# Kernel tuning notes

Measured on AMD Instinct MI355X. Metric: run time of the kernel, lower is better.

The kernel has to match this reference:

```python
import jax, jax.numpy as jnp
import numpy as np

N = 100000   # nodes
E = 1600000  # edges
IN = 768     # in_dim
H = 128      # hidden_dim
G = 64       # graphs per batch


def setup_inputs() -> dict:
    key = jax.random.key(0)
    ks = jax.random.split(key, 9)
    x = jax.random.normal(ks[0], (N, IN), jnp.float32)
    edge_index = jax.random.randint(ks[1], (2, E), 0, N, dtype=jnp.int64)
    batch = jnp.sort(jax.random.randint(ks[2], (N,), 0, G, dtype=jnp.int64))
    W1 = jax.random.normal(ks[3], (IN, H), jnp.float32) / np.float32(np.sqrt(IN))
    b1 = jax.random.normal(ks[4], (H,), jnp.float32) * 0.01
    W2 = jax.random.normal(ks[5], (H, H), jnp.float32) / np.float32(np.sqrt(H))
    b2 = jax.random.normal(ks[6], (H,), jnp.float32) * 0.01
    Wh = jax.random.normal(ks[7], (H, 2), jnp.float32) / np.float32(np.sqrt(H))
    bh = jax.random.normal(ks[8], (2,), jnp.float32) * 0.01
    return dict(x=x, edge_index=edge_index, batch=batch, W1=W1, b1=b1,
                W2=W2, b2=b2, Wh=Wh, bh=bh, num_graphs=G)


def gcn_conv(x, src, dst, W, b, n):
    # PyG GCNConv default: add self-loops (already in src/dst), symmetric norm.
    deg = jax.ops.segment_sum(jnp.ones_like(dst, x.dtype), dst, num_segments=n)
    dis = jnp.where(deg > 0, jax.lax.rsqrt(deg), jnp.zeros_like(deg))
    h = x @ W                                   # [n, out]
    norm = (dis[src] * dis[dst])[:, None]       # [E+n, 1]
    out = jax.ops.segment_sum(h[src] * norm, dst, num_segments=n)
    return out + b


def reference(x, edge_index, batch, W1, b1, W2, b2, Wh, bh, num_graphs):
    n = x.shape[0]
    loop = jnp.arange(n, dtype=edge_index.dtype)
    src = jnp.concatenate([edge_index[0], loop])
    dst = jnp.concatenate([edge_index[1], loop])
    h = jax.nn.relu(gcn_conv(x, src, dst, W1, b1, n))   # dropout = eval identity
    h = jax.nn.relu(gcn_conv(h, src, dst, W2, b2, n))
    summed = jax.ops.segment_sum(h, batch, num_segments=num_graphs)
    counts = jax.ops.segment_sum(jnp.ones((n, 1), h.dtype), batch, num_segments=num_graphs)
    emb = summed / jnp.maximum(counts, 1.0)             # global_mean_pool
    return emb @ Wh + bh
```

## Files before the change

kernel.cpp:

```cpp
#include <hip/hip_runtime.h>
#include <hip/hip_bf16.h>
#include <hip/hip_fp16.h>

static constexpr int N_NODES  = 100000;
static constexpr int N_EDGES  = 1600000;
static constexpr int DIM_IN   = 768;
static constexpr int DIM_H    = 128;
static constexpr int N_GRAPHS = 64;
static constexpr int NB_SCAN  = (N_NODES + 255) / 256;

typedef __attribute__((ext_vector_type(8))) _Float16 half8;
typedef __attribute__((ext_vector_type(4))) float f32x4;

__global__ void k_indeg(const int* __restrict__ edst, int* __restrict__ indeg) {
    int e = blockIdx.x * 256 + threadIdx.x;
    if (e < N_EDGES) atomicAdd(&indeg[edst[e]], 1);
}

__global__ void k_convW(const float* __restrict__ W1, const float* __restrict__ W2,
                        _Float16* __restrict__ W1t, _Float16* __restrict__ W2t) {
    int i = blockIdx.x * 256 + threadIdx.x;
    const int total1 = DIM_IN * DIM_H;
    if (i < total1) {
        int k = i >> 7, n = i & 127;
        W1t[(size_t)n * DIM_IN + k] = (_Float16)W1[i];
    } else if (i < total1 + DIM_H * DIM_H) {
        int j = i - total1;
        int k = j >> 7, n = j & 127;
        W2t[(size_t)n * DIM_H + k] = (_Float16)W2[j];
    }
}

__global__ void k_scan1(const int* __restrict__ indeg, int* __restrict__ rp,
                        int* __restrict__ bsum, float* __restrict__ dis) {
    __shared__ int s[256];
    int t = threadIdx.x;
    int i = blockIdx.x * 256 + t;
    int v = (i < N_NODES) ? indeg[i] : 0;
    s[t] = v;
    __syncthreads();
    for (int off = 1; off < 256; off <<= 1) {
        int x = (t >= off) ? s[t - off] : 0;
        __syncthreads();
        s[t] += x;
        __syncthreads();
    }
    if (i < N_NODES) {
        rp[i] = s[t] - v;
        dis[i] = rsqrtf((float)v + 1.0f);
    }
    if (t == 255) bsum[blockIdx.x] = s[255];
}

__global__ void k_scan2(int* __restrict__ bsum, const int* __restrict__ batch,
                        int* __restrict__ gstart) {
    __shared__ int s[512];
    int t = threadIdx.x;
    int v = (t < NB_SCAN) ? bsum[t] : 0;
    s[t] = v;
    __syncthreads();
    for (int off = 1; off < 512; off <<= 1) {
        int x = (t >= off) ? s[t - off] : 0;
        __syncthreads();
        s[t] += x;
        __syncthreads();
    }
    if (t < NB_SCAN) bsum[t] = s[t] - v;
    if (t <= N_GRAPHS) {
        int lo = 0, hi = N_NODES;
        while (lo < hi) {
            int mid = (lo + hi) >> 1;
            if (batch[mid] < t) lo = mid + 1; else hi = mid;
        }
        gstart[t] = lo;
    }
}

__global__ void k_scatter(const int* __restrict__ esrc, const int* __restrict__ edst,
                          const int* __restrict__ rp, const int* __restrict__ bsum,
                          const float* __restrict__ dis,
                          int* __restrict__ cursor, uint2* __restrict__ csrw) {
    int e = blockIdx.x * 256 + threadIdx.x;
    if (e >= N_EDGES) return;
    int d = edst[e];
    int sv = esrc[e];
    int pos = atomicAdd(&cursor[d], 1);
    uint2 val;
    val.x = (uint)sv;
    val.y = __float_as_uint(dis[sv]);
    csrw[rp[d] + bsum[d >> 8] + pos] = val;
}

#define LDSTR 40

template<int K, bool AFP32>
__global__ __launch_bounds__(256) void k_gemm_mfma(const void* __restrict__ Av,
                                                   const _Float16* __restrict__ Wt,
                                                   _Float16* __restrict__ C,
                                                   int nrows) {
    __shared__ ushort As[128 * LDSTR];
    __shared__ ushort Bs[128 * LDSTR];

    const int t = threadIdx.x;
    const int row0 = blockIdx.x * 128;
    const int srow = t >> 1;
    const int skoff = (t & 1) * 16;
    const int l = t & 63;
    const int wv = t >> 6;
    const int wm = wv >> 1, wn = wv & 1;
    const int lr = l & 15;
    const int lk = (l >> 4) * 8;

    f32x4 acc[4][4];
    const f32x4 zero = {0.f, 0.f, 0.f, 0.f};
    #pragma unroll
    for (int m = 0; m < 4; ++m)
        #pragma unroll
        for (int n = 0; n < 4; ++n) acc[m][n] = zero;

    for (int k0 = 0; k0 < K; k0 += 32) {
        if (AFP32) {
            union { _Float16 h[16]; uint4 q[2]; } cv;
            float f[16];
            if (row0 + srow < nrows) {
                const float4* Ap = (const float4*)((const float*)Av +
                    (size_t)(row0 + srow) * K + k0 + skoff);
                *(float4*)&f[0]  = Ap[0];
                *(float4*)&f[4]  = Ap[1];
                *(float4*)&f[8]  = Ap[2];
                *(float4*)&f[12] = Ap[3];
            } else {
                #pragma unroll
                for (int i = 0; i < 16; ++i) f[i] = 0.f;
            }
            #pragma unroll
            for (int i = 0; i < 16; ++i) cv.h[i] = (_Float16)f[i];
            *(uint4*)&As[srow * LDSTR + skoff]     = cv.q[0];
            *(uint4*)&As[srow * LDSTR + skoff + 8] = cv.q[1];
        } else {
            uint4 q0 = {0, 0, 0, 0}, q1 = {0, 0, 0, 0};
            if (row0 + srow < nrows) {
                const uint4* Ap = (const uint4*)((const _Float16*)Av +
                    (size_t)(row0 + srow) * K + k0 + skoff);
                q0 = Ap[0]; q1 = Ap[1];
            }
            *(uint4*)&As[srow * LDSTR + skoff]     = q0;
            *(uint4*)&As[srow * LDSTR + skoff + 8] = q1;
        }
        {
            const uint4* Wp = (const uint4*)(Wt + (size_t)srow * K + k0 + skoff);
            *(uint4*)&Bs[srow * LDSTR + skoff]     = Wp[0];
            *(uint4*)&Bs[srow * LDSTR + skoff + 8] = Wp[1];
        }
        __syncthreads();

        half8 a[4], b[4];
        #pragma unroll
        for (int m = 0; m < 4; ++m)
            a[m] = *(const half8*)&As[(wm * 64 + m * 16 + lr) * LDSTR + lk];
        #pragma unroll
        for (int n = 0; n < 4; ++n)
            b[n] = *(const half8*)&Bs[(wn * 64 + n * 16 + lr) * LDSTR + lk];
        #pragma unroll
        for (int m = 0; m < 4; ++m)
            #pragma unroll
            for (int n = 0; n < 4; ++n)
                acc[m][n] = __builtin_amdgcn_mfma_f32_16x16x32_f16(a[m], b[n], acc[m][n], 0, 0, 0);
        __syncthreads();
    }

    #pragma unroll
    for (int m = 0; m < 4; ++m) {
        #pragma unroll
        for (int n = 0; n < 4; ++n) {
            int col = wn * 64 + n * 16 + lr;
            #pragma unroll
            for (int j = 0; j < 4; ++j) {
                int row = row0 + wm * 64 + m * 16 + (l >> 4) * 4 + j;
                if (row < nrows)
                    C[(size_t)row * DIM_H + col] = (_Float16)acc[m][n][j];
            }
        }
    }
}

__device__ __forceinline__ void acc8(uint4 u, float w, float* a) {
    __half2 h0 = *(__half2*)&u.x;
    __half2 h1 = *(__half2*)&u.y;
    __half2 h2 = *(__half2*)&u.z;
    __half2 h3 = *(__half2*)&u.w;
    a[0] += __low2float(h0) * w; a[1] += __high2float(h0) * w;
    a[2] += __low2float(h1) * w; a[3] += __high2float(h1) * w;
    a[4] += __low2float(h2) * w; a[5] += __high2float(h2) * w;
    a[6] += __low2float(h3) * w; a[7] += __high2float(h3) * w;
}

__global__ __launch_bounds__(256) void k_agg(const _Float16* __restrict__ hin,
                                             const uint2* __restrict__ csrw,
                                             const int* __restrict__ rp,
                                             const int* __restrict__ bsum,
                                             const int* __restrict__ indeg,
                                             const float* __restrict__ dis,
                                             const float* __restrict__ bias,
                                             _Float16* __restrict__ hout) {
    int node = (blockIdx.x * 256 + threadIdx.x) >> 6;
    int lane = threadIdx.x & 63;
    if (node >= N_NODES) return;
    int q  = lane >> 4;
    int cl = lane & 15;
    float di = dis[node];
    int beg = rp[node] + bsum[node >> 8];
    int cnt = indeg[node];

    float a[8] = {0.f, 0.f, 0.f, 0.f, 0.f, 0.f, 0.f, 0.f};

    {
        uint s; float w;
        if (q == 0)             { s = (uint)node; w = di * di; }
        else if (q - 1 < cnt)   { uint2 p = csrw[beg + q - 1]; s = p.x; w = __uint_as_float(p.y) * di; }
        else                    { s = (uint)node; w = 0.f; }
        uint4 u = ((const uint4*)(hin + (size_t)s * DIM_H))[cl];
        acc8(u, w, a);
    }
    const uint2* cp = csrw + beg + 3;
    int m = cnt - 3;
    int i = 0;
    for (; i + 8 <= m; i += 8) {
        uint2 p0 = cp[i + q];
        uint2 p1 = cp[i + 4 + q];
        float w0 = __uint_as_float(p0.y) * di;
        float w1 = __uint_as_float(p1.y) * di;
        uint4 u0 = ((const uint4*)(hin + (size_t)p0.x * DIM_H))[cl];
        uint4 u1 = ((const uint4*)(hin + (size_t)p1.x * DIM_H))[cl];
        acc8(u0, w0, a);
        acc8(u1, w1, a);
    }
    for (; i < m; i += 4) {
        int idx = i + q;
        uint s; float w;
        if (idx < m) { uint2 p = cp[idx]; s = p.x; w = __uint_as_float(p.y) * di; }
        else         { s = (uint)node;    w = 0.f; }
        uint4 u = ((const uint4*)(hin + (size_t)s * DIM_H))[cl];
        acc8(u, w, a);
    }

    #pragma unroll
    for (int j = 0; j < 8; ++j) {
        a[j] += __shfl_xor(a[j], 16);
        a[j] += __shfl_xor(a[j], 32);
    }

    if (q == 0) {
        float4 b0 = ((const float4*)bias)[cl * 2];
        float4 b1 = ((const float4*)bias)[cl * 2 + 1];
        __half2 h0 = __floats2half2_rn(fmaxf(a[0] + b0.x, 0.f), fmaxf(a[1] + b0.y, 0.f));
        __half2 h1 = __floats2half2_rn(fmaxf(a[2] + b0.z, 0.f), fmaxf(a[3] + b0.w, 0.f));
        __half2 h2 = __floats2half2_rn(fmaxf(a[4] + b1.x, 0.f), fmaxf(a[5] + b1.y, 0.f));
        __half2 h3 = __floats2half2_rn(fmaxf(a[6] + b1.z, 0.f), fmaxf(a[7] + b1.w, 0.f));
        uint4 o;
        o.x = *(uint*)&h0; o.y = *(uint*)&h1; o.z = *(uint*)&h2; o.w = *(uint*)&h3;
        ((uint4*)(hout + (size_t)node * DIM_H))[cl] = o;
    }
}

#define PSPLIT 8
__global__ __launch_bounds__(256) void k_pool(const _Float16* __restrict__ h,
                                              const int* __restrict__ gstart,
                                              float* __restrict__ pooled2) {
    int g  = blockIdx.x >> 3;
    int sp = blockIdx.x & 7;
    int r0 = gstart[g], r1 = gstart[g + 1];
    int count = r1 - r0;
    int chunk = (count + PSPLIT - 1) / PSPLIT;
    int aS = r0 + sp * chunk;
    int bE = min(aS + chunk, r1);
    int c  = threadIdx.x & 63;
    int rr = threadIdx.x >> 6;
    float s0a = 0.f, s1a = 0.f, s0b = 0.f, s1b = 0.f;
    int r = aS + rr;
    for (; r + 4 < bE; r += 8) {
        uint ua = ((const uint*)(h + (size_t)r * DIM_H))[c];
        uint ub = ((const uint*)(h + (size_t)(r + 4) * DIM_H))[c];
        __half2 ha = *(__half2*)&ua;
        __half2 hb = *(__half2*)&ub;
        s0a += __low2float(ha); s1a += __high2float(ha);
        s0b += __low2float(hb); s1b += __high2float(hb);
    }
    if (r < bE) {
        uint ua = ((const uint*)(h + (size_t)r * DIM_H))[c];
        __half2 ha = *(__half2*)&ua;
        s0a += __low2float(ha); s1a += __high2float(ha);
    }
    float s0 = s0a + s0b, s1 = s1a + s1b;
    __shared__ float sm0[4][64], sm1[4][64];
    sm0[rr][c] = s0; sm1[rr][c] = s1;
    __syncthreads();
    if (rr == 0) {
        float v0 = sm0[0][c] + sm0[1][c] + sm0[2][c] + sm0[3][c];
        float v1 = sm1[0][c] + sm1[1][c] + sm1[2][c] + sm1[3][c];
        float* dst = pooled2 + (size_t)(g * PSPLIT + sp) * DIM_H;
        dst[2 * c]     = v0;
        dst[2 * c + 1] = v1;
    }
}

__global__ __launch_bounds__(128) void k_head(const float* __restrict__ pooled2,
                                              const int* __restrict__ gstart,
                                              const float* __restrict__ Wh,
                                              const float* __restrict__ bh,
                                              float* __restrict__ out) {
    int g = blockIdx.x;
    int c = threadIdx.x;
    float s = 0.f;
    #pragma unroll
    for (int sp = 0; sp < PSPLIT; ++sp)
        s += pooled2[(size_t)(g * PSPLIT + sp) * DIM_H + c];
    float cntg = (float)(gstart[g + 1] - gstart[g]);
    float e = s / fmaxf(cntg, 1.0f);
    __shared__ float s0[128], s1[128];
    s0[c] = e * Wh[c * 2 + 0];
    s1[c] = e * Wh[c * 2 + 1];
    __syncthreads();
    for (int off = 64; off > 0; off >>= 1) {
        if (c < off) { s0[c] += s0[c + off]; s1[c] += s1[c + off]; }
        __syncthreads();
    }
    if (c == 0) {
        out[g * 2 + 0] = s0[0] + bh[0];
        out[g * 2 + 1] = s1[0] + bh[1];
    }
}

extern "C" void kernel_launch(void* const* d_in, const int* in_sizes, int n_in,
                              void* d_out, int out_size, void* d_ws, size_t ws_size,
                              hipStream_t stream) {
    const float* x    = (const float*)d_in[0];
    const int*   esrc = (const int*)d_in[1];
    const int*   edst = esrc + N_EDGES;
    const int*   batch= (const int*)d_in[2];
    const float* W1   = (const float*)d_in[3];
    const float* b1   = (const float*)d_in[4];
    const float* W2   = (const float*)d_in[5];
    const float* b2   = (const float*)d_in[6];
    const float* Wh   = (const float*)d_in[7];
    const float* bh   = (const float*)d_in[8];
    float* out = (float*)d_out;

    char* ws = (char*)d_ws;
    size_t off = 0;
    auto alloc = [&](size_t bytes) {
        void* p = ws + off;
        off += (bytes + 255) & ~(size_t)255;
        return p;
    };
    _Float16* bufZ   = (_Float16*)alloc((size_t)N_NODES * DIM_H * 2);
    _Float16* bufH   = (_Float16*)alloc((size_t)N_NODES * DIM_H * 2);
    float*    dis    = (float*)alloc((size_t)N_NODES * 4);
    int*      deg2   = (int*)  alloc((size_t)2 * N_NODES * 4);
    int*      indeg  = deg2;
    int*      cursor = deg2 + N_NODES;
    int*      rp     = (int*)  alloc((size_t)N_NODES * 4);
    uint2*    csrw   = (uint2*)alloc((size_t)N_EDGES * 8);
    int*      bsum   = (int*)  alloc(512 * 4);
    float*    pooled2= (float*)alloc((size_t)N_GRAPHS * PSPLIT * DIM_H * 4);
    int*      gstart = (int*)  alloc((N_GRAPHS + 1) * 4);
    _Float16* W1t    = (_Float16*)alloc((size_t)DIM_IN * DIM_H * 2);
    _Float16* W2t    = (_Float16*)alloc((size_t)DIM_H * DIM_H * 2);

    hipMemsetAsync(deg2, 0, (size_t)2 * N_NODES * 4, stream);

    int convblocks = (DIM_IN * DIM_H + DIM_H * DIM_H + 255) / 256;
    k_convW  <<<convblocks, 256, 0, stream>>>(W1, W2, W1t, W2t);

    k_indeg  <<<(N_EDGES + 255) / 256, 256, 0, stream>>>(edst, indeg);
    k_scan1  <<<NB_SCAN, 256, 0, stream>>>(indeg, rp, bsum, dis);
    k_scan2  <<<1, 512, 0, stream>>>(bsum, batch, gstart);
    k_scatter<<<(N_EDGES + 255) / 256, 256, 0, stream>>>(esrc, edst, rp, bsum, dis, cursor, csrw);

    int gblocks = (N_NODES + 127) / 128;
    k_gemm_mfma<DIM_IN, true ><<<gblocks, 256, 0, stream>>>(x,    W1t, bufZ, N_NODES);
    k_agg<<<(N_NODES + 3) / 4, 256, 0, stream>>>(bufZ, csrw, rp, bsum, indeg, dis, b1, bufH);
    k_gemm_mfma<DIM_H,  false><<<gblocks, 256, 0, stream>>>(bufH, W2t, bufZ, N_NODES);
    k_agg<<<(N_NODES + 3) / 4, 256, 0, stream>>>(bufZ, csrw, rp, bsum, indeg, dis, b2, bufH);

    k_pool<<<N_GRAPHS * PSPLIT, 256, 0, stream>>>(bufH, gstart, pooled2);
    k_head<<<N_GRAPHS, 128, 0, stream>>>(pooled2, gstart, Wh, bh, out);
}
```

Baseline: 441.5 us.

## Prefetch GEMM tiles into registers, batch aggregation gathers, fuse preprocessing kernels

Measured after the change: 511.3 us. 1.16x slower.

```diff
diff --git a/kernel.cpp b/kernel.cpp
--- a/kernel.cpp
+++ b/kernel.cpp
@@ -12,14 +12,11 @@
 typedef __attribute__((ext_vector_type(8))) _Float16 half8;
 typedef __attribute__((ext_vector_type(4))) float f32x4;
 
-__global__ void k_indeg(const int* __restrict__ edst, int* __restrict__ indeg) {
-    int e = blockIdx.x * 256 + threadIdx.x;
-    if (e < N_EDGES) atomicAdd(&indeg[edst[e]], 1);
-}
-
-__global__ void k_convW(const float* __restrict__ W1, const float* __restrict__ W2,
-                        _Float16* __restrict__ W1t, _Float16* __restrict__ W2t) {
+__global__ void k_pre(const int* __restrict__ edst, int* __restrict__ indeg,
+                      const float* __restrict__ W1, const float* __restrict__ W2,
+                      _Float16* __restrict__ W1t, _Float16* __restrict__ W2t) {
     int i = blockIdx.x * 256 + threadIdx.x;
+    if (i < N_EDGES) atomicAdd(&indeg[edst[i]], 1);
     const int total1 = DIM_IN * DIM_H;
     if (i < total1) {
         int k = i >> 7, n = i & 127;
@@ -110,6 +107,7 @@
     const int wm = wv >> 1, wn = wv & 1;
     const int lr = l & 15;
     const int lk = (l >> 4) * 8;
+    const bool arow_ok = (row0 + srow < nrows);
 
     f32x4 acc[4][4];
     const f32x4 zero = {0.f, 0.f, 0.f, 0.f};
@@ -118,40 +116,56 @@
         #pragma unroll
         for (int n = 0; n < 4; ++n) acc[m][n] = zero;
 
+    float4 fa[4];
+    uint4  ha[2];
+    uint4  wq[2];
+
+    auto loadA = [&](int k0) {
+        if (AFP32) {
+            if (arow_ok) {
+                const float4* p = (const float4*)((const float*)Av +
+                    (size_t)(row0 + srow) * K + k0 + skoff);
+                fa[0] = p[0]; fa[1] = p[1]; fa[2] = p[2]; fa[3] = p[3];
+            } else {
+                float4 z = {0.f, 0.f, 0.f, 0.f};
+                fa[0] = z; fa[1] = z; fa[2] = z; fa[3] = z;
+            }
+        } else {
+            if (arow_ok) {
+                const uint4* p = (const uint4*)((const _Float16*)Av +
+                    (size_t)(row0 + srow) * K + k0 + skoff);
+                ha[0] = p[0]; ha[1] = p[1];
+            } else {
+                uint4 z = {0, 0, 0, 0};
+                ha[0] = z; ha[1] = z;
+            }
+        }
+    };
+    auto loadW = [&](int k0) {
+        const uint4* p = (const uint4*)(Wt + (size_t)srow * K + k0 + skoff);
+        wq[0] = p[0]; wq[1] = p[1];
+    };
+
+    loadA(0); loadW(0);
     for (int k0 = 0; k0 < K; k0 += 32) {
         if (AFP32) {
             union { _Float16 h[16]; uint4 q[2]; } cv;
-            float f[16];
-            if (row0 + srow < nrows) {
-                const float4* Ap = (const float4*)((const float*)Av +
-                    (size_t)(row0 + srow) * K + k0 + skoff);
-                *(float4*)&f[0]  = Ap[0];
-                *(float4*)&f[4]  = Ap[1];
-                *(float4*)&f[8]  = Ap[2];
-                *(float4*)&f[12] = Ap[3];
-            } else {
-                #pragma unroll
-                for (int i = 0; i < 16; ++i) f[i] = 0.f;
+            #pragma unroll
+            for (int i = 0; i < 4; ++i) {
+                cv.h[4 * i + 0] = (_Float16)fa[i].x;
+                cv.h[4 * i + 1] = (_Float16)fa[i].y;
+                cv.h[4 * i + 2] = (_Float16)fa[i].z;
+                cv.h[4 * i + 3] = (_Float16)fa[i].w;
             }
-            #pragma unroll
-            for (int i = 0; i < 16; ++i) cv.h[i] = (_Float16)f[i];
             *(uint4*)&As[srow * LDSTR + skoff]     = cv.q[0];
             *(uint4*)&As[srow * LDSTR + skoff + 8] = cv.q[1];
         } else {
-            uint4 q0 = {0, 0, 0, 0}, q1 = {0, 0, 0, 0};
-            if (row0 + srow < nrows) {
-                const uint4* Ap = (const uint4*)((const _Float16*)Av +
-                    (size_t)(row0 + srow) * K + k0 + skoff);
-                q0 = Ap[0]; q1 = Ap[1];
-            }
-            *(uint4*)&As[srow * LDSTR + skoff]     = q0;
-            *(uint4*)&As[srow * LDSTR + skoff + 8] = q1;
-        }
-        {
-            const uint4* Wp = (const uint4*)(Wt + (size_t)srow * K + k0 + skoff);
-            *(uint4*)&Bs[srow * LDSTR + skoff]     = Wp[0];
-            *(uint4*)&Bs[srow * LDSTR + skoff + 8] = Wp[1];
-        }
+            *(uint4*)&As[srow * LDSTR + skoff]     = ha[0];
+            *(uint4*)&As[srow * LDSTR + skoff + 8] = ha[1];
+        }
+        *(uint4*)&Bs[srow * LDSTR + skoff]     = wq[0];
+        *(uint4*)&Bs[srow * LDSTR + skoff + 8] = wq[1];
+        if (k0 + 32 < K) { loadA(k0 + 32); loadW(k0 + 32); }
         __syncthreads();
 
         half8 a[4], b[4];
@@ -209,39 +223,32 @@
     int q  = lane >> 4;
     int cl = lane & 15;
     float di = dis[node];
+    uint dibits = __float_as_uint(di);
     int beg = rp[node] + bsum[node >> 8];
     int cnt = indeg[node];
+    int T = cnt + 1;
 
     float a[8] = {0.f, 0.f, 0.f, 0.f, 0.f, 0.f, 0.f, 0.f};
 
-    {
-        uint s; float w;
-        if (q == 0)             { s = (uint)node; w = di * di; }
-        else if (q - 1 < cnt)   { uint2 p = csrw[beg + q - 1]; s = p.x; w = __uint_as_float(p.y) * di; }
-        else                    { s = (uint)node; w = 0.f; }
-        uint4 u = ((const uint4*)(hin + (size_t)s * DIM_H))[cl];
-        acc8(u, w, a);
-    }
-    const uint2* cp = csrw + beg + 3;
-    int m = cnt - 3;
-    int i = 0;
-    for (; i + 8 <= m; i += 8) {
-        uint2 p0 = cp[i + q];
-        uint2 p1 = cp[i + 4 + q];
-        float w0 = __uint_as_float(p0.y) * di;
-        float w1 = __uint_as_float(p1.y) * di;
-        uint4 u0 = ((const uint4*)(hin + (size_t)p0.x * DIM_H))[cl];
-        uint4 u1 = ((const uint4*)(hin + (size_t)p1.x * DIM_H))[cl];
-        acc8(u0, w0, a);
-        acc8(u1, w1, a);
-    }
-    for (; i < m; i += 4) {
-        int idx = i + q;
-        uint s; float w;
-        if (idx < m) { uint2 p = cp[idx]; s = p.x; w = __uint_as_float(p.y) * di; }
-        else         { s = (uint)node;    w = 0.f; }
-        uint4 u = ((const uint4*)(hin + (size_t)s * DIM_H))[cl];
-        acc8(u, w, a);
+    for (int base = 0; base < T; base += 32) {
+        uint2 ps[8];
+        #pragma unroll
+        for (int j = 0; j < 8; ++j) {
+            int idx = base + j * 4 + q;
+            int ci = min(idx, T - 1);
+            int ei = min(beg + max(ci, 1) - 1, N_EDGES - 1);
+            uint2 pv = csrw[ei];
+            if (ci == 0)  { pv.x = (uint)node; pv.y = dibits; }
+            if (idx >= T) { pv.x = (uint)node; pv.y = 0u; }
+            ps[j] = pv;
+        }
+        uint4 us[8];
+        #pragma unroll
+        for (int j = 0; j < 8; ++j)
+            us[j] = ((const uint4*)(hin + (size_t)ps[j].x * DIM_H))[cl];
+        #pragma unroll
+        for (int j = 0; j < 8; ++j)
+            acc8(us[j], __uint_as_float(ps[j].y) * di, a);
     }
 
     #pragma unroll
@@ -369,10 +376,7 @@
 
     hipMemsetAsync(deg2, 0, (size_t)2 * N_NODES * 4, stream);
 
-    int convblocks = (DIM_IN * DIM_H + DIM_H * DIM_H + 255) / 256;
-    k_convW  <<<convblocks, 256, 0, stream>>>(W1, W2, W1t, W2t);
-
-    k_indeg  <<<(N_EDGES + 255) / 256, 256, 0, stream>>>(edst, indeg);
+    k_pre    <<<(N_EDGES + 255) / 256, 256, 0, stream>>>(edst, indeg, W1, W2, W1t, W2t);
     k_scan1  <<<NB_SCAN, 256, 0, stream>>>(indeg, rp, bsum, dis);
     k_scan2  <<<1, 512, 0, stream>>>(bsum, batch, gstart);
     k_scatter<<<(N_EDGES + 255) / 256, 256, 0, stream>>>(esrc, edst, rp, bsum, dis, cursor, csrw);
```
